# Optimization experiments

Measured on AMD Instinct MI355X. Metric: run time of the kernel, lower is better.

Reference implementation:

```python
import math
import jax, jax.numpy as jnp
from jax import lax
import numpy as np

B, C, H, W = 2, 48, 64, 64
DI, DS, DCONV, DTR = 96, 16, 4, 3   # d_inner=expand*dim, d_state, d_conv, dt_rank=ceil(48/16)
HF = 96                              # SEFN hidden = dim * ffn_expansion_factor(2)


def _posenc(L, d):
    pos = jnp.arange(L, dtype=jnp.float32)[:, None]
    div = jnp.exp(jnp.arange(0, d, 2, dtype=jnp.float32) * (-math.log(10000.0) / d))
    pe = jnp.zeros((L, d), jnp.float32)
    pe = pe.at[:, 0::2].set(jnp.sin(pos * div))
    pe = pe.at[:, 1::2].set(jnp.cos(pos * div))
    return pe


def _ln(x, w, b, eps=1e-5):  # last-dim LayerNorm, biased variance (torch unbiased=False)
    mu = x.mean(-1, keepdims=True)
    var = ((x - mu) ** 2).mean(-1, keepdims=True)
    return (x - mu) / jnp.sqrt(var + eps) * w + b


def _ln4d(x, w, b):  # WithBias LayerNorm over channel dim of NCHW (to_3d/to_4d round trip)
    b_, c_, h_, w_ = x.shape
    xf = x.reshape(b_, c_, h_ * w_).transpose(0, 2, 1)
    return _ln(xf, w, b).transpose(0, 2, 1).reshape(b_, c_, h_, w_)


def _flip_odd(x):  # flip last axis on odd rows of axis -2 (snake reordering)
    return x.at[:, :, 1::2, :].set(x[:, :, 1::2, ::-1])


def _conv2d(x, w, bias=None, groups=1, pad=0):
    y = lax.conv_general_dilated(x, w, (1, 1), [(pad, pad), (pad, pad)],
                                 feature_group_count=groups,
                                 dimension_numbers=('NCHW', 'OIHW', 'NCHW'))
    if bias is not None:
        y = y + bias[None, :, None, None]
    return y


def _mamba(x, inproj, convw, convb, xproj, dtw, dtb, Alog, D, outproj):
    # standard mamba_ssm Mamba forward; x: (B, L, C)
    b_, L, _ = x.shape
    xz = x @ inproj.T                      # (B, L, 2*DI)
    xm, z = xz[..., :DI], xz[..., DI:]
    xc = xm.transpose(0, 2, 1)             # (B, DI, L)
    xc = lax.conv_general_dilated(xc, convw, (1,), [(DCONV - 1, 0)],
                                  feature_group_count=DI,
                                  dimension_numbers=('NCH', 'OIH', 'NCH'))
    xc = jax.nn.silu(xc + convb[None, :, None]).transpose(0, 2, 1)  # (B, L, DI)
    x_dbl = xc @ xproj.T                   # (B, L, DTR + 2*DS)
    dt = jax.nn.softplus(x_dbl[..., :DTR] @ dtw.T + dtb)            # (B, L, DI)
    Bm = x_dbl[..., DTR:DTR + DS]          # (B, L, DS)
    Cm = x_dbl[..., DTR + DS:]             # (B, L, DS)
    A = -jnp.exp(Alog)                     # (DI, DS)
    dA = jnp.exp(dt[..., None] * A)        # (B, L, DI, DS)
    dBx = dt[..., None] * Bm[:, :, None, :] * xc[..., None]

    def step(h, t):
        dA_t, dBx_t, C_t = t
        h = dA_t * h + dBx_t
        return h, jnp.einsum('bds,bs->bd', h, C_t)

    h0 = jnp.zeros((b_, DI, DS), x.dtype)
    _, ys = lax.scan(step, h0, (dA.transpose(1, 0, 2, 3), dBx.transpose(1, 0, 2, 3), Cm.transpose(1, 0, 2)))
    y = ys.transpose(1, 0, 2) + xc * D
    y = y * jax.nn.silu(z)
    return y @ outproj.T


def _forward(x, n1_w, n1_b, n2_w, n2_b, mln1_w, mln1_b, mln2_w, mln2_b,
             m1, m2, f_pin, f_dw, f_fus, f_dwa, f_pout,
             f_c1w, f_c1b, f_ln1_w, f_ln1_b, f_c2w, f_c2b, f_ln2_w, f_ln2_b):
    x_spatial = x
    L = H * W
    pe = _posenc(L, C)
    # --- MambaLayer: bidirectional flip-scan ---
    xn = _ln4d(x, n1_w, n1_b)
    rev1 = _flip_odd(xn)                               # snake order over rows
    rev2 = _flip_odd(xn.transpose(0, 1, 3, 2))         # snake order over cols
    x1_flat = rev1.reshape(B, C, L).transpose(0, 2, 1) + pe
    x2_flat = rev2.reshape(B, C, L).transpose(0, 2, 1) + pe
    y1 = _mamba(_ln(x1_flat, mln1_w, mln1_b), *m1)
    y2 = _mamba(_ln(x2_flat, mln2_w, mln2_b), *m2)
    out1 = _flip_odd(y1.transpose(0, 2, 1).reshape(B, C, H, W))
    out2 = _flip_odd(y2.transpose(0, 2, 1).reshape(B, C, W, H)).transpose(0, 1, 3, 2)
    x = x + out1 + out2
    # --- SEFN ---
    xn2 = _ln4d(x, n2_w, n2_b)
    xp = _conv2d(xn2, f_pin)                           # (B, 2*HF, H, W)
    y = x_spatial.reshape(B, C, H // 2, 2, W // 2, 2).mean((3, 5))   # AvgPool2d(2)
    y = jax.nn.relu(_ln4d(_conv2d(y, f_c1w, f_c1b, pad=1), f_ln1_w, f_ln1_b))
    y = jax.nn.relu(_ln4d(_conv2d(y, f_c2w, f_c2b, pad=1), f_ln2_w, f_ln2_b))
    y = jnp.repeat(jnp.repeat(y, 2, axis=2), 2, axis=3)              # nearest Upsample(2)
    xd = _conv2d(xp, f_dw, groups=2 * HF, pad=1)
    x1, x2 = xd[:, :HF], xd[:, HF:]
    x1 = _conv2d(jnp.concatenate([x1, y], axis=1), f_fus)
    x1 = _conv2d(x1, f_dwa, groups=HF, pad=1)
    ff = _conv2d(jax.nn.gelu(x1, approximate=False) * x2, f_pout)
    return x + ff


def setup_inputs():
    key = jax.random.key(0)
    ks = iter(jax.random.split(key, 64))

    def nrm(shape, s):
        return s * jax.random.normal(next(ks), shape, jnp.float32)

    inp = {}
    inp['x'] = nrm((B, C, H, W), 1.0)
    for nm in ['n1', 'n2', 'mln1', 'mln2', 'f_ln1', 'f_ln2']:
        inp[nm + '_w'] = jnp.ones((C,), jnp.float32)
        inp[nm + '_b'] = jnp.zeros((C,), jnp.float32)
    for p in ['m1', 'm2']:
        inp[p + '_inproj'] = nrm((2 * DI, C), 0.1)
        inp[p + '_convw'] = nrm((DI, 1, DCONV), 0.3)
        inp[p + '_convb'] = jnp.zeros((DI,), jnp.float32)
        inp[p + '_xproj'] = nrm((DTR + 2 * DS, DI), 0.1)
        inp[p + '_dtw'] = nrm((DI, DTR), 0.3)
        u = jax.random.uniform(next(ks), (DI,), jnp.float32)
        inp[p + '_dtb'] = jnp.log(jnp.expm1(0.001 + 0.099 * u))  # mamba dt bias init
        inp[p + '_Alog'] = jnp.log(jnp.tile(jnp.arange(1., DS + 1., dtype=jnp.float32), (DI, 1)))
        inp[p + '_D'] = jnp.ones((DI,), jnp.float32)
        inp[p + '_outproj'] = nrm((C, DI), 0.1)
    inp['f_pin'] = nrm((2 * HF, C, 1, 1), 0.1)
    inp['f_dw'] = nrm((2 * HF, 1, 3, 3), 0.2)
    inp['f_fus'] = nrm((HF, HF + C, 1, 1), 0.08)
    inp['f_dwa'] = nrm((HF, 1, 3, 3), 0.2)
    inp['f_pout'] = nrm((C, HF, 1, 1), 0.1)
    inp['f_c1w'] = nrm((C, C, 3, 3), 0.05)
    inp['f_c1b'] = jnp.zeros((C,), jnp.float32)
    inp['f_c2w'] = nrm((C, C, 3, 3), 0.05)
    inp['f_c2b'] = jnp.zeros((C,), jnp.float32)
    return inp


def reference(x, n1_w, n1_b, n2_w, n2_b, mln1_w, mln1_b, mln2_w, mln2_b,
              m1_inproj, m1_convw, m1_convb, m1_xproj, m1_dtw, m1_dtb, m1_Alog, m1_D, m1_outproj,
              m2_inproj, m2_convw, m2_convb, m2_xproj, m2_dtw, m2_dtb, m2_Alog, m2_D, m2_outproj,
              f_pin, f_dw, f_fus, f_dwa, f_pout,
              f_c1w, f_c1b, f_ln1_w, f_ln1_b, f_c2w, f_c2b, f_ln2_w, f_ln2_b):
    m1 = (m1_inproj, m1_convw, m1_convb, m1_xproj, m1_dtw, m1_dtb, m1_Alog, m1_D, m1_outproj)
    m2 = (m2_inproj, m2_convw, m2_convb, m2_xproj, m2_dtw, m2_dtb, m2_Alog, m2_D, m2_outproj)
    return _forward(x, n1_w, n1_b, n2_w, n2_b, mln1_w, mln1_b, mln2_w, mln2_b,
                    m1, m2, f_pin, f_dw, f_fus, f_dwa, f_pout,
                    f_c1w, f_c1b, f_ln1_w, f_ln1_b, f_c2w, f_c2b, f_ln2_w, f_ln2_b)
```

## Files before the change

### kernel.cpp

```cpp
#include <hip/hip_runtime.h>

#define DEV __device__ __forceinline__

DEV float siluf(float x){ return x / (1.f + __expf(-x)); }
DEV float softplusf(float x){ return fmaxf(x, 0.f) + log1pf(expf(-fabsf(x))); }
DEV float geluf(float x){ return 0.5f * x * (1.f + erff(x * 0.70710678118654752440f)); }

__global__ __launch_bounds__(256) void kA_front(const float* __restrict__ x,
    const float* __restrict__ n1w, const float* __restrict__ n1b,
    const float* __restrict__ mw0, const float* __restrict__ mb0,
    const float* __restrict__ mw1, const float* __restrict__ mb1,
    const float* __restrict__ ip0, const float* __restrict__ ip1,
    float* __restrict__ xmg, float* __restrict__ Vg){
  __shared__ alignas(16) float Vl[48*36];
  __shared__ float Wt[48*97];
  __shared__ float mu_s[32], rs_s[32];
  int bd = blockIdx.x >> 7, tile = blockIdx.x & 127;
  int dir = bd >> 1, b = bd & 1;
  int t0 = tile*32;
  int tid = threadIdx.x;
  const float* ip = dir ? ip1 : ip0;
  const float* mw = dir ? mw1 : mw0;
  const float* mb = dir ? mb1 : mb0;
  for (int i = tid; i < 96*48; i += 256){
    int j = i / 48, c = i % 48;
    Wt[c*97 + j] = ip[i];
  }
  for (int i = tid; i < 48*32; i += 256){
    int c = i >> 5, r = i & 31;
    int t = t0 + r;
    int h, w;
    if (dir == 0){ h = t >> 6; int wp = t & 63; w = (h & 1) ? 63 - wp : wp; }
    else         { w = t >> 6; int hp = t & 63; h = (w & 1) ? 63 - hp : hp; }
    Vl[c*36 + r] = x[(size_t)b*48*4096 + c*4096 + h*64 + w];
  }
  __syncthreads();
  {
    int r = tid >> 3, k = tid & 7;
    float s1 = 0.f, s2 = 0.f;
    #pragma unroll
    for (int cc = 0; cc < 6; cc++){
      float v = Vl[(k*6+cc)*36 + r];
      s1 += v; s2 += v*v;
    }
    s1 += __shfl_xor(s1,1); s2 += __shfl_xor(s2,1);
    s1 += __shfl_xor(s1,2); s2 += __shfl_xor(s2,2);
    s1 += __shfl_xor(s1,4); s2 += __shfl_xor(s2,4);
    if (k == 0){
      float m = s1*(1.f/48.f);
      mu_s[r] = m;
      rs_s[r] = rsqrtf(s2*(1.f/48.f) - m*m + 1e-5f);
    }
  }
  __syncthreads();
  for (int i = tid; i < 32*48; i += 256){
    int r = i / 48, c = i % 48;
    int t = t0 + r;
    float v = Vl[c*36 + r];
    float xn = (v - mu_s[r])*rs_s[r]*n1w[c] + n1b[c];
    float ang = (float)t * __expf(-(float)(c & ~1) * (9.210340371976184f/48.f));
    float pe = (c & 1) ? cosf(ang) : sinf(ang);
    Vl[c*36 + r] = xn + pe;
  }
  __syncthreads();
  {
    int r = tid >> 3, k = tid & 7;
    float s1 = 0.f, s2 = 0.f;
    #pragma unroll
    for (int cc = 0; cc < 6; cc++){
      float v = Vl[(k*6+cc)*36 + r];
      s1 += v; s2 += v*v;
    }
    s1 += __shfl_xor(s1,1); s2 += __shfl_xor(s2,1);
    s1 += __shfl_xor(s1,2); s2 += __shfl_xor(s2,2);
    s1 += __shfl_xor(s1,4); s2 += __shfl_xor(s2,4);
    if (k == 0){
      float m = s1*(1.f/48.f);
      mu_s[r] = m;
      rs_s[r] = rsqrtf(s2*(1.f/48.f) - m*m + 1e-5f);
    }
  }
  __syncthreads();
  for (int i = tid; i < 32*48; i += 256){
    int r = i / 48, c = i % 48;
    float v = Vl[c*36 + r];
    float v2 = (v - mu_s[r])*rs_s[r]*mw[c] + mb[c];
    Vl[c*36 + r] = v2;
    Vg[((size_t)bd*4096 + t0 + r)*48 + c] = v2;
  }
  __syncthreads();
  for (int k = 0; k < 3; k++){
    int i = tid + k*256;
    int j = i % 96, rb = i / 96;
    float a0=0.f, a1=0.f, a2=0.f, a3=0.f;
    #pragma unroll 4
    for (int c = 0; c < 48; c++){
      float wv = Wt[c*97 + j];
      const float4 v4 = *(const float4*)&Vl[c*36 + rb*4];
      a0 += wv*v4.x; a1 += wv*v4.y; a2 += wv*v4.z; a3 += wv*v4.w;
    }
    size_t g = ((size_t)bd*4096 + t0 + rb*4)*96 + j;
    xmg[g] = a0; xmg[g+96] = a1; xmg[g+192] = a2; xmg[g+288] = a3;
  }
}

__global__ __launch_bounds__(384) void kB_convscan(const float* __restrict__ xmg,
    const float* __restrict__ cwp0, const float* __restrict__ cwp1,
    const float* __restrict__ cbp0, const float* __restrict__ cbp1,
    const float* __restrict__ xpp0, const float* __restrict__ xpp1,
    const float* __restrict__ dwp0, const float* __restrict__ dwp1,
    const float* __restrict__ dbp0, const float* __restrict__ dbp1,
    const float* __restrict__ Alog0, const float* __restrict__ Alog1,
    float* __restrict__ xcg, float* __restrict__ dtg,
    float* __restrict__ Bmg, float* __restrict__ Cmg,
    float* __restrict__ P, float* __restrict__ S){
  __shared__ union UB {
    float xml[96*36];
    struct { float xwl[35*96]; float xdbl[35*33]; } p;
  } ub;
  __shared__ float xcl[96*33];
  __shared__ float dtl[96*33];
  __shared__ alignas(16) float Bl[32*16], Cl[32*16];
  __shared__ float cw[96*4], cbv[96], dwl[96*3], dbl[96];
  int bd = blockIdx.x >> 7, tile = blockIdx.x & 127;
  int dir = bd >> 1;
  int t0 = tile*32;
  int tid = threadIdx.x;
  const float* cwp = dir ? cwp1 : cwp0;
  const float* cbp = dir ? cbp1 : cbp0;
  const float* xpp = dir ? xpp1 : xpp0;
  const float* dwp = dir ? dwp1 : dwp0;
  const float* dbp = dir ? dbp1 : dbp0;
  const float* Alog = dir ? Alog1 : Alog0;
  for (int i = tid; i < 35*96; i += 384){
    int tl = i / 96, d = i % 96;
    int t = t0 - 3 + tl;
    ub.xml[d*36 + tl] = (t >= 0) ? xmg[((size_t)bd*4096 + t)*96 + d] : 0.f;
  }
  for (int i = tid; i < 96*4;  i += 384) cw[i] = cwp[i];
  for (int i = tid; i < 96*3;  i += 384) dwl[i] = dwp[i];
  for (int i = tid; i < 96;    i += 384){ cbv[i] = cbp[i]; dbl[i] = dbp[i]; }
  __syncthreads();
  for (int i = tid; i < 96*32; i += 384){
    int d = i >> 5, t = i & 31;
    float acc = cbv[d];
    #pragma unroll
    for (int k = 0; k < 4; k++) acc += cw[d*4+k]*ub.xml[d*36 + t + k];
    xcl[d*33 + t] = siluf(acc);
  }
  __syncthreads();
  for (int i = tid; i < 35*96; i += 384) ub.p.xwl[i] = xpp[i];
  __syncthreads();
  for (int i = tid; i < 35*32; i += 384){
    int j = i / 32, t = i % 32;
    float acc = 0.f;
    #pragma unroll 4
    for (int d = 0; d < 96; d++) acc += xcl[d*33 + t]*ub.p.xwl[j*96 + d];
    ub.p.xdbl[j*33 + t] = acc;
  }
  __syncthreads();
  for (int i = tid; i < 96*32; i += 384){
    int d = i >> 5, t = i & 31;
    float v = dbl[d];
    #pragma unroll
    for (int r = 0; r < 3; r++) v += ub.p.xdbl[r*33 + t]*dwl[d*3 + r];
    dtl[d*33 + t] = softplusf(v);
  }
  for (int i = tid; i < 32*16; i += 384){
    int t = i / 16, s = i % 16;
    Bl[t*16 + s] = ub.p.xdbl[(3+s)*33 + t];
    Cl[t*16 + s] = ub.p.xdbl[(19+s)*33 + t];
  }
  __syncthreads();
  for (int i = tid; i < 32*96; i += 384){
    int t = i / 96, d = i % 96;
    size_t g = ((size_t)bd*4096 + t0 + t)*96 + d;
    xcg[g] = xcl[d*33 + t];
    dtg[g] = dtl[d*33 + t];
  }
  for (int i = tid; i < 32*16; i += 384){
    int t = i / 16, s = i % 16;
    size_t g = ((size_t)bd*4096 + t0 + t)*16 + s;
    Bmg[g] = Bl[t*16 + s];
    Cmg[g] = Cl[t*16 + s];
  }
  {
    int d = tid >> 2, q = tid & 3;
    float A0 = -__expf(Alog[d*16 + q*4 + 0]);
    float A1 = -__expf(Alog[d*16 + q*4 + 1]);
    float A2 = -__expf(Alog[d*16 + q*4 + 2]);
    float A3 = -__expf(Alog[d*16 + q*4 + 3]);
    float h0=0.f,h1=0.f,h2=0.f,h3=0.f, p0=1.f,p1=1.f,p2=1.f,p3=1.f;
    #pragma unroll 4
    for (int t = 0; t < 32; t++){
      float dtd = dtl[d*33 + t];
      float u = dtd * xcl[d*33 + t];
      const float4 b4 = *(const float4*)&Bl[t*16 + q*4];
      float a0 = __expf(dtd*A0), a1 = __expf(dtd*A1), a2 = __expf(dtd*A2), a3 = __expf(dtd*A3);
      h0 = a0*h0 + u*b4.x; p0 *= a0;
      h1 = a1*h1 + u*b4.y; p1 *= a1;
      h2 = a2*h2 + u*b4.z; p2 *= a2;
      h3 = a3*h3 + u*b4.w; p3 *= a3;
    }
    size_t ob = (size_t)blockIdx.x*1536 + d*16 + q*4;
    *(float4*)&P[ob] = make_float4(p0,p1,p2,p3);
    *(float4*)&S[ob] = make_float4(h0,h1,h2,h3);
  }
}

__global__ __launch_bounds__(256) void k4_comb(float* __restrict__ P, const float* __restrict__ S){
  int tid2 = blockIdx.x*256 + threadIdx.x;
  int bd = tid2 / 1536, r = tid2 % 1536;
  size_t idx = (size_t)bd*128*1536 + r;
  const int ST = 1536;
  float pb0,pb1,pb2,pb3,pb4,pb5,pb6,pb7, sb0,sb1,sb2,sb3,sb4,sb5,sb6,sb7;
  pb0=P[idx+0*ST]; sb0=S[idx+0*ST]; pb1=P[idx+1*ST]; sb1=S[idx+1*ST];
  pb2=P[idx+2*ST]; sb2=S[idx+2*ST]; pb3=P[idx+3*ST]; sb3=S[idx+3*ST];
  pb4=P[idx+4*ST]; sb4=S[idx+4*ST]; pb5=P[idx+5*ST]; sb5=S[idx+5*ST];
  pb6=P[idx+6*ST]; sb6=S[idx+6*ST]; pb7=P[idx+7*ST]; sb7=S[idx+7*ST];
  float h = 0.f;
  for (int c0 = 0; c0 < 128; c0 += 8){
    float pn0=0,sn0=0,pn1=0,sn1=0,pn2=0,sn2=0,pn3=0,sn3=0;
    float pn4=0,sn4=0,pn5=0,sn5=0,pn6=0,sn6=0,pn7=0,sn7=0;
    if (c0 + 8 < 128){
      pn0=P[idx+(size_t)(c0+8)*ST];  sn0=S[idx+(size_t)(c0+8)*ST];
      pn1=P[idx+(size_t)(c0+9)*ST];  sn1=S[idx+(size_t)(c0+9)*ST];
      pn2=P[idx+(size_t)(c0+10)*ST]; sn2=S[idx+(size_t)(c0+10)*ST];
      pn3=P[idx+(size_t)(c0+11)*ST]; sn3=S[idx+(size_t)(c0+11)*ST];
      pn4=P[idx+(size_t)(c0+12)*ST]; sn4=S[idx+(size_t)(c0+12)*ST];
      pn5=P[idx+(size_t)(c0+13)*ST]; sn5=S[idx+(size_t)(c0+13)*ST];
      pn6=P[idx+(size_t)(c0+14)*ST]; sn6=S[idx+(size_t)(c0+14)*ST];
      pn7=P[idx+(size_t)(c0+15)*ST]; sn7=S[idx+(size_t)(c0+15)*ST];
    }
    P[idx+(size_t)(c0+0)*ST] = h; h = pb0*h + sb0;
    P[idx+(size_t)(c0+1)*ST] = h; h = pb1*h + sb1;
    P[idx+(size_t)(c0+2)*ST] = h; h = pb2*h + sb2;
    P[idx+(size_t)(c0+3)*ST] = h; h = pb3*h + sb3;
    P[idx+(size_t)(c0+4)*ST] = h; h = pb4*h + sb4;
    P[idx+(size_t)(c0+5)*ST] = h; h = pb5*h + sb5;
    P[idx+(size_t)(c0+6)*ST] = h; h = pb6*h + sb6;
    P[idx+(size_t)(c0+7)*ST] = h; h = pb7*h + sb7;
    pb0=pn0;sb0=sn0;pb1=pn1;sb1=sn1;pb2=pn2;sb2=sn2;pb3=pn3;sb3=sn3;
    pb4=pn4;sb4=sn4;pb5=pn5;sb5=sn5;pb6=pn6;sb6=sn6;pb7=pn7;sb7=sn7;
  }
}

__global__ __launch_bounds__(384) void k5_scan2(const float* __restrict__ dtg,
    const float* __restrict__ xcg, const float* __restrict__ Bmg, const float* __restrict__ Cmg,
    const float* __restrict__ Alog0, const float* __restrict__ Alog1,
    const float* __restrict__ Dp0, const float* __restrict__ Dp1,
    const float* __restrict__ ip0, const float* __restrict__ ip1,
    const float* __restrict__ Vg, const float* __restrict__ Hin, float* __restrict__ yout){
  __shared__ union U5 {
    struct { float dts[32*96]; float xcs[32*96]; } s;
    struct { float Wzt[48*96]; float Vgs[32*48]; } e;
  } u;
  __shared__ alignas(16) float Bl[32*16], Cl[32*16];
  __shared__ float yl[32*96];
  int task = blockIdx.x;
  int bd = task >> 7, ch = task & 127;
  int t0 = ch*32;
  int tid = threadIdx.x;
  const float* ip   = (bd >= 2) ? ip1 : ip0;
  const float* Alog = (bd >= 2) ? Alog1 : Alog0;
  const float* Dp   = (bd >= 2) ? Dp1 : Dp0;
  for (int i = tid; i < 32*96; i += 384){
    int t = i / 96, dd = i % 96;
    size_t g = ((size_t)bd*4096 + t0 + t)*96 + dd;
    u.s.dts[i] = dtg[g];
    u.s.xcs[i] = xcg[g];
  }
  for (int i = tid; i < 32*16; i += 384){
    size_t g = ((size_t)bd*4096 + t0)*16 + i;
    Bl[i] = Bmg[g];
    Cl[i] = Cmg[g];
  }
  __syncthreads();
  {
    int d = tid >> 2, q = tid & 3;
    float A0 = -__expf(Alog[d*16 + q*4 + 0]);
    float A1 = -__expf(Alog[d*16 + q*4 + 1]);
    float A2 = -__expf(Alog[d*16 + q*4 + 2]);
    float A3 = -__expf(Alog[d*16 + q*4 + 3]);
    float Dd = Dp[d];
    const float4 h4 = *(const float4*)&Hin[(size_t)task*1536 + d*16 + q*4];
    float h0 = h4.x, h1 = h4.y, h2 = h4.z, h3 = h4.w;
    for (int t = 0; t < 32; t += 2){
      float dtdA = u.s.dts[t*96 + d];
      float xcvA = u.s.xcs[t*96 + d];
// ... 69 lines not shown
    if (pass == 0){
      for (int i = tid; i < 16*96; i += 384){
        int wl_ = i / 96, d = i % 96;
        int wsp = w0 + wl_;
        int wp = (h & 1) ? 63 - wsp : wsp;
        ul.ylds[wl_*97 + d] = y[((size_t)b*4096 + h*64 + wp)*96 + d];
      }
    } else {
      for (int i = tid; i < 16*96; i += 384){
        int wl_ = i / 96, d = i % 96;
        int wsp = w0 + wl_;
        int t = wsp*64 + ((wsp & 1) ? 63 - h : h);
        ul.ylds[wl_*97 + d] = y[((size_t)b*4096 + t)*96 + d];
      }
    }
    __syncthreads();
    #pragma unroll 4
    for (int d = 0; d < 96; d++){
      float yv = ul.ylds[w*97 + d];
      acc0 += yv * bufW[(cg*2+0)*97 + d];
      acc1 += yv * bufW[(cg*2+1)*97 + d];
    }
  }
  __syncthreads();
  {
    int c0 = cg*2;
    size_t idx0 = (((size_t)b*48 + c0)*64 + h)*64 + w0 + w;
    float v0 = x[idx0] + acc0;
    xmid[idx0] = v0;
    ul.l.xl[c0*17 + w] = v0;
    size_t idx1 = idx0 + 4096;
    float v1 = x[idx1] + acc1;
    xmid[idx1] = v1;
    ul.l.xl[(c0+1)*17 + w] = v1;
  }
  for (int i = tid; i < 192*48; i += 384){
    int r = i / 48, c = i % 48;
    bufW[r*49 + c] = pin[i];
  }
  __syncthreads();
  if (tid < 128){
    int r = tid >> 3, k = tid & 7;
    float s1 = 0.f, s2 = 0.f;
    #pragma unroll
    for (int cc = 0; cc < 6; cc++){
      float v = ul.l.xl[(k*6+cc)*17 + r];
      s1 += v; s2 += v*v;
    }
    s1 += __shfl_xor(s1,1); s2 += __shfl_xor(s2,1);
    s1 += __shfl_xor(s1,2); s2 += __shfl_xor(s2,2);
    s1 += __shfl_xor(s1,4); s2 += __shfl_xor(s2,4);
    if (k == 0){
      float m = s1*(1.f/48.f);
      ul.l.mu[r] = m;
      ul.l.rs[r] = rsqrtf(s2*(1.f/48.f) - m*m + 1e-5f);
    }
  }
  __syncthreads();
  for (int i = tid; i < 48*16; i += 384){
    int c = i >> 4, ww = i & 15;
    ul.l.xl[c*17 + ww] = (ul.l.xl[c*17 + ww] - ul.l.mu[ww])*ul.l.rs[ww]*nw[c] + nb[c];
  }
  __syncthreads();
  for (int it = 0; it < 2; it++){
    int i = tid + it*384;
    int ww = i & 15, oq = i >> 4;
    int o0 = oq*4;
    float a0=0,a1=0,a2=0,a3=0;
    #pragma unroll 4
    for (int c = 0; c < 48; c++){
      float xv = ul.l.xl[c*17 + ww];
      a0 += xv*bufW[(o0+0)*49 + c];
      a1 += xv*bufW[(o0+1)*49 + c];
      a2 += xv*bufW[(o0+2)*49 + c];
      a3 += xv*bufW[(o0+3)*49 + c];
    }
    xp[(((size_t)b*192 + o0+0)*64 + h)*64 + w0 + ww] = a0;
    xp[(((size_t)b*192 + o0+1)*64 + h)*64 + w0 + ww] = a1;
    xp[(((size_t)b*192 + o0+2)*64 + h)*64 + w0 + ww] = a2;
    xp[(((size_t)b*192 + o0+3)*64 + h)*64 + w0 + ww] = a3;
  }
}

__global__ __launch_bounds__(384) void k9_conv3(const float* __restrict__ in,
    const float* __restrict__ wgt, const float* __restrict__ bias,
    const float* __restrict__ lnw, const float* __restrict__ lnb,
    float* __restrict__ out, int pooled, int lnin){
  __shared__ float wl[12*48*9];
  __shared__ float sin_[48*3*34];
  __shared__ float mu_i[104], rs_i[104];
  int bid = blockIdx.x;
  int cq = bid & 3, i0 = (bid >> 2) & 31, b = bid >> 7;
  int tid = threadIdx.x;
  for (int i = tid; i < 12*48*9; i += 384) wl[i] = wgt[cq*12*48*9 + i];
  for (int i = tid; i < 48*3*34; i += 384){
    int jx = i % 34, ky = (i/34) % 3, ci = i/102;
    int r = i0 + ky - 1, j = jx - 1;
    float v = 0.f;
    if (r >= 0 && r < 32 && j >= 0 && j < 32){
      if (pooled){
        const float* xb = in + (((size_t)b*48 + ci)*64 + 2*r)*64 + 2*j;
        v = 0.25f*(xb[0] + xb[1] + xb[64] + xb[65]);
      } else {
        v = in[(((size_t)b*48 + ci)*32 + r)*32 + j];
      }
    }
    sin_[i] = v;
  }
  __syncthreads();
  if (lnin){
    if (tid < 102){
      int jx = tid % 34, ky = tid / 34;
      int r = i0 + ky - 1, j = jx - 1;
      if (r >= 0 && r < 32 && j >= 0 && j < 32){
        float s1 = 0.f, s2 = 0.f;
        #pragma unroll 4
        for (int ci = 0; ci < 48; ci++){ float v = sin_[ci*102 + tid]; s1 += v; s2 += v*v; }
        float m = s1*(1.f/48.f);
        mu_i[tid] = m;
        rs_i[tid] = rsqrtf(s2*(1.f/48.f) - m*m + 1e-5f);
      }
    }
    __syncthreads();
    for (int i = tid; i < 48*102; i += 384){
      int ci = i / 102, p = i % 102;
      int jx = p % 34, ky = p / 34;
      int r = i0 + ky - 1, j = jx - 1;
      if (r >= 0 && r < 32 && j >= 0 && j < 32){
        float v = (sin_[i] - mu_i[p])*rs_i[p]*lnw[ci] + lnb[ci];
        sin_[i] = fmaxf(v, 0.f);
      }
    }
    __syncthreads();
  }
  int j = tid & 31, col = tid >> 5;
  float acc = bias[cq*12 + col];
  for (int ci = 0; ci < 48; ci++){
    const float* wp = wl + ((size_t)col*48 + ci)*9;
    const float* sp = sin_ + ci*102;
    #pragma unroll
    for (int ky = 0; ky < 3; ky++)
      #pragma unroll
      for (int kx = 0; kx < 3; kx++)
        acc += sp[ky*34 + j + kx] * wp[ky*3 + kx];
  }
  out[(((size_t)b*48 + cq*12 + col)*32 + i0)*32 + j] = acc;
}

__global__ __launch_bounds__(256) void k13_dw(const float* __restrict__ in,
    const float* __restrict__ wgt, float* __restrict__ out, int CH){
  int idx = blockIdx.x*256 + threadIdx.x;
  if (idx >= 2*CH*1024) return;
  int wq = idx & 15, h = (idx >> 4) & 63, c = (idx >> 10) % CH, b = idx / (CH*1024);
  int w0 = wq*4;
  const float* ip = in + ((size_t)b*CH + c)*4096;
  const float* wp = wgt + c*9;
  float a0=0.f,a1=0.f,a2=0.f,a3=0.f;
  #pragma unroll
  for (int ky = 0; ky < 3; ky++){
    int hh = h + ky - 1;
    if (hh < 0 || hh > 63) continue;
    const float* rp = ip + hh*64;
    float v0 = (w0 > 0)  ? rp[w0-1] : 0.f;
    float v1 = rp[w0+0], v2 = rp[w0+1], v3 = rp[w0+2], v4 = rp[w0+3];
    float v5 = (w0 < 60) ? rp[w0+4] : 0.f;
    float k0 = wp[ky*3+0], k1 = wp[ky*3+1], k2 = wp[ky*3+2];
    a0 += k0*v0 + k1*v1 + k2*v2;
    a1 += k0*v1 + k1*v2 + k2*v3;
    a2 += k0*v2 + k1*v3 + k2*v4;
    a3 += k0*v3 + k1*v4 + k2*v5;
  }
  float* op = out + (((size_t)b*CH + c)*64 + h)*64 + w0;
  op[0]=a0; op[1]=a1; op[2]=a2; op[3]=a3;
}

__global__ __launch_bounds__(256) void k14_fus(const float* __restrict__ xd,
    const float* __restrict__ cv2, const float* __restrict__ lnw, const float* __restrict__ lnb,
    const float* __restrict__ fus, float* __restrict__ x1){
  __shared__ float wl[48*144];
  __shared__ float al[96][64];
  __shared__ float yl[48][32];
  __shared__ float muy[32], rsy[32];
  int bid = blockIdx.x;
  int oh = bid & 1, h = (bid >> 1) & 63, b = bid >> 7;
  int tid = threadIdx.x;
  for (int i = tid; i < 48*144; i += 256) wl[i] = fus[(size_t)oh*48*144 + i];
  for (int i = tid; i < 96*64; i += 256){
    int ci = i >> 6, w = i & 63;
    al[ci][w] = xd[(((size_t)b*192 + ci)*64 + h)*64 + w];
  }
  for (int i = tid; i < 48*32; i += 256){
    int cj = i >> 5, j = i & 31;
    yl[cj][j] = cv2[(((size_t)b*48 + cj)*32 + (h >> 1))*32 + j];
  }
  __syncthreads();
  if (tid < 32){
    float s1 = 0.f, s2 = 0.f;
    #pragma unroll 4
    for (int cj = 0; cj < 48; cj++){ float v = yl[cj][tid]; s1 += v; s2 += v*v; }
    float m = s1*(1.f/48.f);
    muy[tid] = m;
    rsy[tid] = rsqrtf(s2*(1.f/48.f) - m*m + 1e-5f);
  }
  __syncthreads();
  for (int i = tid; i < 48*32; i += 256){
    int cj = i >> 5, j = i & 31;
    yl[cj][j] = fmaxf((yl[cj][j] - muy[j])*rsy[j]*lnw[cj] + lnb[cj], 0.f);
  }
  __syncthreads();
  for (int it = 0; it < 3; it++){
    int i = tid + it*256;
    int w = i & 63, ob = i >> 6; int o0 = ob*4;
    float a[4] = {0,0,0,0};
    #pragma unroll 4
    for (int ci = 0; ci < 96; ci++){
      float xv = al[ci][w];
      #pragma unroll
      for (int q = 0; q < 4; q++) a[q] += xv * wl[(o0+q)*144 + ci];
    }
    int w2 = w >> 1;
    #pragma unroll 4
    for (int cj = 0; cj < 48; cj++){
      float yv = yl[cj][w2];
      #pragma unroll
      for (int q = 0; q < 4; q++) a[q] += yv * wl[(o0+q)*144 + 96 + cj];
    }
    #pragma unroll
    for (int q = 0; q < 4; q++)
      x1[(((size_t)b*96 + oh*48 + o0 + q)*64 + h)*64 + w] = a[q];
  }
}
// ... 20 lines not shown
    float v = 0.f;
    if (hh >= 0 && hh < 64 && ww_ >= 0 && ww_ < 64)
      v = x1[(((size_t)b*96 + ch)*64 + hh)*64 + ww_];
    xs[i] = v;
  }
  __syncthreads();
  for (int i = tid; i < 96*16; i += 384){
    int ch = i >> 4, ww = i & 15;
    const float* wp = dwl + ch*9;
    const float* sp = xs + ch*54;
    float a = 0.f;
    #pragma unroll
    for (int ky = 0; ky < 3; ky++)
      #pragma unroll
      for (int kx = 0; kx < 3; kx++)
        a += sp[ky*18 + ww + kx] * wp[ky*3 + kx];
    float x2 = xd[(((size_t)b*192 + 96 + ch)*64 + h)*64 + w0 + ww];
    gl[ch*17 + ww] = geluf(a) * x2;
  }
  __syncthreads();
  int ww = tid & 15, cg = tid >> 4;
  float a0=0.f, a1=0.f;
  #pragma unroll 4
  for (int ch = 0; ch < 96; ch++){
    float gv = gl[ch*17 + ww];
    a0 += gv * wl[(cg*2+0)*97 + ch];
    a1 += gv * wl[(cg*2+1)*97 + ch];
  }
  {
    int c0 = cg*2;
    size_t idx0 = (((size_t)b*48 + c0)*64 + h)*64 + w0 + ww;
    out[idx0] = xmid[idx0] + a0;
    size_t idx1 = idx0 + 4096;
    out[idx1] = xmid[idx1] + a1;
  }
}

extern "C" void kernel_launch(void* const* d_in, const int* in_sizes, int n_in,
                              void* d_out, int out_size, void* d_ws, size_t ws_size,
                              hipStream_t stream){
  (void)in_sizes; (void)n_in; (void)out_size; (void)ws_size;
  const float* x    = (const float*)d_in[0];
  const float* n1w  = (const float*)d_in[1];
  const float* n1b  = (const float*)d_in[2];
  const float* n2w  = (const float*)d_in[3];
  const float* n2b  = (const float*)d_in[4];
  const float* mlnw[2] = {(const float*)d_in[5], (const float*)d_in[7]};
  const float* mlnb[2] = {(const float*)d_in[6], (const float*)d_in[8]};
  const float* fln1w = (const float*)d_in[9];
  const float* fln1b = (const float*)d_in[10];
  const float* fln2w = (const float*)d_in[11];
  const float* fln2b = (const float*)d_in[12];
  const float* inproj[2]  = {(const float*)d_in[13], (const float*)d_in[22]};
  const float* convw[2]   = {(const float*)d_in[14], (const float*)d_in[23]};
  const float* convb[2]   = {(const float*)d_in[15], (const float*)d_in[24]};
  const float* xproj[2]   = {(const float*)d_in[16], (const float*)d_in[25]};
  const float* dtw[2]     = {(const float*)d_in[17], (const float*)d_in[26]};
  const float* dtbp[2]    = {(const float*)d_in[18], (const float*)d_in[27]};
  const float* Alog[2]    = {(const float*)d_in[19], (const float*)d_in[28]};
  const float* Dp[2]      = {(const float*)d_in[20], (const float*)d_in[29]};
  const float* outproj[2] = {(const float*)d_in[21], (const float*)d_in[30]};
  const float* fpin  = (const float*)d_in[31];
  const float* fdw   = (const float*)d_in[32];
  const float* ffus  = (const float*)d_in[33];
  const float* fdwa  = (const float*)d_in[34];
  const float* fpout = (const float*)d_in[35];
  const float* fc1w  = (const float*)d_in[36];
  const float* fc1b  = (const float*)d_in[37];
  const float* fc2w  = (const float*)d_in[38];
  const float* fc2b  = (const float*)d_in[39];

  float* ws = (float*)d_ws;
  float* xmg = ws + 0;
  float* Vgb = ws + 1572864;
  float* xcg = ws + 2359296;
  float* dtg = ws + 3932160;
  float* Bmg = ws + 5505024;
  float* Cmg = ws + 5767168;
  float* Pb  = ws + 6029312;
  float* Sb  = ws + 6815744;
  float* xmid= ws + 7602176;
  float* yall = xmg;
  float* Hin  = Pb;
  float* ta   = Sb;
  float* tbuf = Sb + 98304;
  float* xpb  = xcg;
  float* xdb  = dtg;
  float* x1b  = Pb;

  kA_front<<<512,256,0,stream>>>(x, n1w, n1b,
      mlnw[0], mlnb[0], mlnw[1], mlnb[1], inproj[0], inproj[1], xmg, Vgb);
  kB_convscan<<<512,384,0,stream>>>(xmg,
      convw[0], convw[1], convb[0], convb[1], xproj[0], xproj[1],
      dtw[0], dtw[1], dtbp[0], dtbp[1], Alog[0], Alog[1],
      xcg, dtg, Bmg, Cmg, Pb, Sb);
  k4_comb  <<<24,256,0,stream>>>(Pb, Sb);
  k5_scan2 <<<512,384,0,stream>>>(dtg, xcg, Bmg, Cmg, Alog[0], Alog[1],
      Dp[0], Dp[1], inproj[0], inproj[1], Vgb, Hin, yall);
  k67_mid  <<<512,384,0,stream>>>(x, yall, yall + 786432, outproj[0], outproj[1],
      n2w, n2b, fpin, xmid, xpb);
  k9_conv3 <<<256,384,0,stream>>>(x,  fc1w, fc1b, fln1w, fln1b, ta,   1, 0);
  k9_conv3 <<<256,384,0,stream>>>(ta, fc2w, fc2b, fln1w, fln1b, tbuf, 0, 1);
  k13_dw   <<<1536,256,0,stream>>>(xpb, fdw, xdb, 192);
  k14_fus  <<<256,256,0,stream>>>(xdb, tbuf, fln2w, fln2b, ffus, x1b);
  k16_out  <<<512,384,0,stream>>>(x1b, xdb, fdwa, fpout, xmid, (float*)d_out);
}
```

Measured before the change: 184.8 us.

## Merge independent SEFN 3x3 conv branches into the Mamba front kernels

The two 3x3 conv launches on the pooled spatial branch are folded into the Mamba front and conv-scan kernels as extra blocks selected by block index, since they are independent of the Mamba path. This removes two kernel launches and lets the small 256-block conv work overlap with the 512-block Mamba stages. Their intermediate buffers now live in the output buffer instead of the workspace. Shared memory is unioned across roles, and the conv1 branch runs with 256 threads and loops over its 384 outputs.

```diff
diff --git a/kernel.cpp b/kernel.cpp
--- a/kernel.cpp
+++ b/kernel.cpp
@@ -6,205 +6,291 @@
 DEV float softplusf(float x){ return fmaxf(x, 0.f) + log1pf(expf(-fabsf(x))); }
 DEV float geluf(float x){ return 0.5f * x * (1.f + erff(x * 0.70710678118654752440f)); }
 
-__global__ __launch_bounds__(256) void kA_front(const float* __restrict__ x,
+__global__ __launch_bounds__(256) void kA9(const float* __restrict__ x,
     const float* __restrict__ n1w, const float* __restrict__ n1b,
     const float* __restrict__ mw0, const float* __restrict__ mb0,
     const float* __restrict__ mw1, const float* __restrict__ mb1,
     const float* __restrict__ ip0, const float* __restrict__ ip1,
-    float* __restrict__ xmg, float* __restrict__ Vg){
-  __shared__ alignas(16) float Vl[48*36];
-  __shared__ float Wt[48*97];
-  __shared__ float mu_s[32], rs_s[32];
-  int bd = blockIdx.x >> 7, tile = blockIdx.x & 127;
-  int dir = bd >> 1, b = bd & 1;
-  int t0 = tile*32;
+    const float* __restrict__ fc1w, const float* __restrict__ fc1b,
+    float* __restrict__ xmg, float* __restrict__ Vg, float* __restrict__ ta){
+  __shared__ union alignas(16) UA {
+    struct { float Vl[48*36]; float Wt[48*97]; float mu_s[32]; float rs_s[32]; } a;
+    struct { float wl[12*48*9]; float sin_[48*102]; } c;
+  } u;
   int tid = threadIdx.x;
-  const float* ip = dir ? ip1 : ip0;
-  const float* mw = dir ? mw1 : mw0;
-  const float* mb = dir ? mb1 : mb0;
-  for (int i = tid; i < 96*48; i += 256){
-    int j = i / 48, c = i % 48;
-    Wt[c*97 + j] = ip[i];
-  }
-  for (int i = tid; i < 48*32; i += 256){
-    int c = i >> 5, r = i & 31;
-    int t = t0 + r;
-    int h, w;
-    if (dir == 0){ h = t >> 6; int wp = t & 63; w = (h & 1) ? 63 - wp : wp; }
-    else         { w = t >> 6; int hp = t & 63; h = (w & 1) ? 63 - hp : hp; }
-    Vl[c*36 + r] = x[(size_t)b*48*4096 + c*4096 + h*64 + w];
-  }
-  __syncthreads();
-  {
-    int r = tid >> 3, k = tid & 7;
-    float s1 = 0.f, s2 = 0.f;
-    #pragma unroll
-    for (int cc = 0; cc < 6; cc++){
-      float v = Vl[(k*6+cc)*36 + r];
-      s1 += v; s2 += v*v;
-    }
-    s1 += __shfl_xor(s1,1); s2 += __shfl_xor(s2,1);
-    s1 += __shfl_xor(s1,2); s2 += __shfl_xor(s2,2);
-    s1 += __shfl_xor(s1,4); s2 += __shfl_xor(s2,4);
-    if (k == 0){
-      float m = s1*(1.f/48.f);
-      mu_s[r] = m;
-      rs_s[r] = rsqrtf(s2*(1.f/48.f) - m*m + 1e-5f);
-    }
-  }
-  __syncthreads();
-  for (int i = tid; i < 32*48; i += 256){
-    int r = i / 48, c = i % 48;
-    int t = t0 + r;
-    float v = Vl[c*36 + r];
-    float xn = (v - mu_s[r])*rs_s[r]*n1w[c] + n1b[c];
-    float ang = (float)t * __expf(-(float)(c & ~1) * (9.210340371976184f/48.f));
-    float pe = (c & 1) ? cosf(ang) : sinf(ang);
-    Vl[c*36 + r] = xn + pe;
-  }
-  __syncthreads();
-  {
-    int r = tid >> 3, k = tid & 7;
-    float s1 = 0.f, s2 = 0.f;
-    #pragma unroll
-    for (int cc = 0; cc < 6; cc++){
-      float v = Vl[(k*6+cc)*36 + r];
-      s1 += v; s2 += v*v;
-    }
-    s1 += __shfl_xor(s1,1); s2 += __shfl_xor(s2,1);
-    s1 += __shfl_xor(s1,2); s2 += __shfl_xor(s2,2);
-    s1 += __shfl_xor(s1,4); s2 += __shfl_xor(s2,4);
-    if (k == 0){
-      float m = s1*(1.f/48.f);
-      mu_s[r] = m;
-      rs_s[r] = rsqrtf(s2*(1.f/48.f) - m*m + 1e-5f);
-    }
-  }
-  __syncthreads();
-  for (int i = tid; i < 32*48; i += 256){
-    int r = i / 48, c = i % 48;
-    float v = Vl[c*36 + r];
-    float v2 = (v - mu_s[r])*rs_s[r]*mw[c] + mb[c];
-    Vl[c*36 + r] = v2;
-    Vg[((size_t)bd*4096 + t0 + r)*48 + c] = v2;
-  }
-  __syncthreads();
-  for (int k = 0; k < 3; k++){
-    int i = tid + k*256;
-    int j = i % 96, rb = i / 96;
-    float a0=0.f, a1=0.f, a2=0.f, a3=0.f;
-    #pragma unroll 4
-    for (int c = 0; c < 48; c++){
-      float wv = Wt[c*97 + j];
-      const float4 v4 = *(const float4*)&Vl[c*36 + rb*4];
-      a0 += wv*v4.x; a1 += wv*v4.y; a2 += wv*v4.z; a3 += wv*v4.w;
-    }
-    size_t g = ((size_t)bd*4096 + t0 + rb*4)*96 + j;
-    xmg[g] = a0; xmg[g+96] = a1; xmg[g+192] = a2; xmg[g+288] = a3;
-  }
-}
-
-__global__ __launch_bounds__(384) void kB_convscan(const float* __restrict__ xmg,
+  if (blockIdx.x < 512){
+    int bd = blockIdx.x >> 7, tile = blockIdx.x & 127;
+    int dir = bd >> 1, b = bd & 1;
+    int t0 = tile*32;
+    const float* ip = dir ? ip1 : ip0;
+    const float* mw = dir ? mw1 : mw0;
+    const float* mb = dir ? mb1 : mb0;
+    for (int i = tid; i < 96*48; i += 256){
+      int j = i / 48, c = i % 48;
+      u.a.Wt[c*97 + j] = ip[i];
+    }
+    for (int i = tid; i < 48*32; i += 256){
+      int c = i >> 5, r = i & 31;
+      int t = t0 + r;
+      int h, w;
+      if (dir == 0){ h = t >> 6; int wp = t & 63; w = (h & 1) ? 63 - wp : wp; }
+      else         { w = t >> 6; int hp = t & 63; h = (w & 1) ? 63 - hp : hp; }
+      u.a.Vl[c*36 + r] = x[(size_t)b*48*4096 + c*4096 + h*64 + w];
+    }
+    __syncthreads();
+    {
+      int r = tid >> 3, k = tid & 7;
+      float s1 = 0.f, s2 = 0.f;
+      #pragma unroll
+      for (int cc = 0; cc < 6; cc++){
+        float v = u.a.Vl[(k*6+cc)*36 + r];
+        s1 += v; s2 += v*v;
+      }
+      s1 += __shfl_xor(s1,1); s2 += __shfl_xor(s2,1);
+      s1 += __shfl_xor(s1,2); s2 += __shfl_xor(s2,2);
+      s1 += __shfl_xor(s1,4); s2 += __shfl_xor(s2,4);
+      if (k == 0){
+        float m = s1*(1.f/48.f);
+        u.a.mu_s[r] = m;
+        u.a.rs_s[r] = rsqrtf(s2*(1.f/48.f) - m*m + 1e-5f);
+      }
+    }
+    __syncthreads();
+    for (int i = tid; i < 32*48; i += 256){
+      int r = i / 48, c = i % 48;
+      int t = t0 + r;
+      float v = u.a.Vl[c*36 + r];
+      float xn = (v - u.a.mu_s[r])*u.a.rs_s[r]*n1w[c] + n1b[c];
+      float ang = (float)t * __expf(-(float)(c & ~1) * (9.210340371976184f/48.f));
+      float pe = (c & 1) ? cosf(ang) : sinf(ang);
+      u.a.Vl[c*36 + r] = xn + pe;
+    }
+    __syncthreads();
+    {
+      int r = tid >> 3, k = tid & 7;
+      float s1 = 0.f, s2 = 0.f;
+      #pragma unroll
+      for (int cc = 0; cc < 6; cc++){
+        float v = u.a.Vl[(k*6+cc)*36 + r];
+        s1 += v; s2 += v*v;
+      }
+      s1 += __shfl_xor(s1,1); s2 += __shfl_xor(s2,1);
+      s1 += __shfl_xor(s1,2); s2 += __shfl_xor(s2,2);
+      s1 += __shfl_xor(s1,4); s2 += __shfl_xor(s2,4);
+      if (k == 0){
+        float m = s1*(1.f/48.f);
+        u.a.mu_s[r] = m;
+        u.a.rs_s[r] = rsqrtf(s2*(1.f/48.f) - m*m + 1e-5f);
+      }
+    }
+    __syncthreads();
+    for (int i = tid; i < 32*48; i += 256){
+      int r = i / 48, c = i % 48;
+      float v = u.a.Vl[c*36 + r];
+      float v2 = (v - u.a.mu_s[r])*u.a.rs_s[r]*mw[c] + mb[c];
+      u.a.Vl[c*36 + r] = v2;
+      Vg[((size_t)bd*4096 + t0 + r)*48 + c] = v2;
+    }
+    __syncthreads();
+    for (int k = 0; k < 3; k++){
+      int i = tid + k*256;
+      int j = i % 96, rb = i / 96;
+      float a0=0.f, a1=0.f, a2=0.f, a3=0.f;
+      #pragma unroll 4
+      for (int c = 0; c < 48; c++){
+        float wv = u.a.Wt[c*97 + j];
+        const float4 v4 = *(const float4*)&u.a.Vl[c*36 + rb*4];
+        a0 += wv*v4.x; a1 += wv*v4.y; a2 += wv*v4.z; a3 += wv*v4.w;
+      }
+      size_t g = ((size_t)bd*4096 + t0 + rb*4)*96 + j;
+      xmg[g] = a0; xmg[g+96] = a1; xmg[g+192] = a2; xmg[g+288] = a3;
+    }
+  } else {
+    int bid = blockIdx.x - 512;
+    int cq = bid & 3, i0 = (bid >> 2) & 31, b2 = bid >> 7;
+    for (int i = tid; i < 12*48*9; i += 256) u.c.wl[i] = fc1w[cq*12*48*9 + i];
+    for (int i = tid; i < 48*102; i += 256){
+      int jx = i % 34, ky = (i/34) % 3, ci = i/102;
+      int r = i0 + ky - 1, j = jx - 1;
+      float v = 0.f;
+      if (r >= 0 && r < 32 && j >= 0 && j < 32){
+        const float* xb = x + (((size_t)b2*48 + ci)*64 + 2*r)*64 + 2*j;
+        v = 0.25f*(xb[0] + xb[1] + xb[64] + xb[65]);
+      }
+      u.c.sin_[i] = v;
+    }
+    __syncthreads();
+    for (int i = tid; i < 12*32; i += 256){
+      int j = i & 31, col = i >> 5;
+      float acc = fc1b[cq*12 + col];
+      for (int ci = 0; ci < 48; ci++){
+        const float* wp = u.c.wl + ((size_t)col*48 + ci)*9;
+        const float* sp = u.c.sin_ + ci*102;
+        #pragma unroll
+        for (int ky = 0; ky < 3; ky++)
+          #pragma unroll
+          for (int kx = 0; kx < 3; kx++)
+            acc += sp[ky*34 + j + kx] * wp[ky*3 + kx];
+      }
+      ta[(((size_t)b2*48 + cq*12 + col)*32 + i0)*32 + j] = acc;
+    }
+  }
+}
+
+__global__ __launch_bounds__(384) void kB9(const float* __restrict__ xmg,
     const float* __restrict__ cwp0, const float* __restrict__ cwp1,
     const float* __restrict__ cbp0, const float* __restrict__ cbp1,
     const float* __restrict__ xpp0, const float* __restrict__ xpp1,
     const float* __restrict__ dwp0, const float* __restrict__ dwp1,
     const float* __restrict__ dbp0, const float* __restrict__ dbp1,
     const float* __restrict__ Alog0, const float* __restrict__ Alog1,
+    const float* __restrict__ ta, const float* __restrict__ fc2w, const float* __restrict__ fc2b,
+    const float* __restrict__ fln1w, const float* __restrict__ fln1b,
     float* __restrict__ xcg, float* __restrict__ dtg,
     float* __restrict__ Bmg, float* __restrict__ Cmg,
-    float* __restrict__ P, float* __restrict__ S){
-  __shared__ union UB {
-    float xml[96*36];
-    struct { float xwl[35*96]; float xdbl[35*33]; } p;
-  } ub;
-  __shared__ float xcl[96*33];
-  __shared__ float dtl[96*33];
-  __shared__ alignas(16) float Bl[32*16], Cl[32*16];
-  __shared__ float cw[96*4], cbv[96], dwl[96*3], dbl[96];
-  int bd = blockIdx.x >> 7, tile = blockIdx.x & 127;
-  int dir = bd >> 1;
-  int t0 = tile*32;
+    float* __restrict__ P, float* __restrict__ S, float* __restrict__ tbuf){
+  __shared__ union alignas(16) UBB {
+    struct {
+      float Bl[32*16]; float Cl[32*16];
+      union { float xml[96*36]; struct { float xwl[35*96]; float xdbl[35*33]; } p; } ub;
+      float xcl[96*33]; float dtl[96*33];
+      float cw[96*4]; float cbv[96]; float dwl[96*3]; float dbl[96];
+    } b;
+    struct { float wl[12*48*9]; float sin_[48*102]; float mu_i[104]; float rs_i[104]; } c;
+  } u;
   int tid = threadIdx.x;
-  const float* cwp = dir ? cwp1 : cwp0;
-  const float* cbp = dir ? cbp1 : cbp0;
-  const float* xpp = dir ? xpp1 : xpp0;
-  const float* dwp = dir ? dwp1 : dwp0;
-  const float* dbp = dir ? dbp1 : dbp0;
-  const float* Alog = dir ? Alog1 : Alog0;
-  for (int i = tid; i < 35*96; i += 384){
-    int tl = i / 96, d = i % 96;
-    int t = t0 - 3 + tl;
-    ub.xml[d*36 + tl] = (t >= 0) ? xmg[((size_t)bd*4096 + t)*96 + d] : 0.f;
-  }
-  for (int i = tid; i < 96*4;  i += 384) cw[i] = cwp[i];
-  for (int i = tid; i < 96*3;  i += 384) dwl[i] = dwp[i];
-  for (int i = tid; i < 96;    i += 384){ cbv[i] = cbp[i]; dbl[i] = dbp[i]; }
-  __syncthreads();
-  for (int i = tid; i < 96*32; i += 384){
-    int d = i >> 5, t = i & 31;
-    float acc = cbv[d];
-    #pragma unroll
-    for (int k = 0; k < 4; k++) acc += cw[d*4+k]*ub.xml[d*36 + t + k];
-    xcl[d*33 + t] = siluf(acc);
-  }
-  __syncthreads();
-  for (int i = tid; i < 35*96; i += 384) ub.p.xwl[i] = xpp[i];
-  __syncthreads();
-  for (int i = tid; i < 35*32; i += 384){
-    int j = i / 32, t = i % 32;
-    float acc = 0.f;
-    #pragma unroll 4
-    for (int d = 0; d < 96; d++) acc += xcl[d*33 + t]*ub.p.xwl[j*96 + d];
-    ub.p.xdbl[j*33 + t] = acc;
-  }
-  __syncthreads();
-  for (int i = tid; i < 96*32; i += 384){
-    int d = i >> 5, t = i & 31;
-    float v = dbl[d];
-    #pragma unroll
-    for (int r = 0; r < 3; r++) v += ub.p.xdbl[r*33 + t]*dwl[d*3 + r];
-    dtl[d*33 + t] = softplusf(v);
-  }
-  for (int i = tid; i < 32*16; i += 384){
-    int t = i / 16, s = i % 16;
-    Bl[t*16 + s] = ub.p.xdbl[(3+s)*33 + t];
-    Cl[t*16 + s] = ub.p.xdbl[(19+s)*33 + t];
-  }
-  __syncthreads();
-  for (int i = tid; i < 32*96; i += 384){
-    int t = i / 96, d = i % 96;
-    size_t g = ((size_t)bd*4096 + t0 + t)*96 + d;
-    xcg[g] = xcl[d*33 + t];
-    dtg[g] = dtl[d*33 + t];
-  }
-  for (int i = tid; i < 32*16; i += 384){
-    int t = i / 16, s = i % 16;
-    size_t g = ((size_t)bd*4096 + t0 + t)*16 + s;
-    Bmg[g] = Bl[t*16 + s];
-    Cmg[g] = Cl[t*16 + s];
-  }
-  {
-    int d = tid >> 2, q = tid & 3;
-    float A0 = -__expf(Alog[d*16 + q*4 + 0]);
-    float A1 = -__expf(Alog[d*16 + q*4 + 1]);
-    float A2 = -__expf(Alog[d*16 + q*4 + 2]);
-    float A3 = -__expf(Alog[d*16 + q*4 + 3]);
-    float h0=0.f,h1=0.f,h2=0.f,h3=0.f, p0=1.f,p1=1.f,p2=1.f,p3=1.f;
-    #pragma unroll 4
-    for (int t = 0; t < 32; t++){
-      float dtd = dtl[d*33 + t];
-      float u = dtd * xcl[d*33 + t];
-      const float4 b4 = *(const float4*)&Bl[t*16 + q*4];
-      float a0 = __expf(dtd*A0), a1 = __expf(dtd*A1), a2 = __expf(dtd*A2), a3 = __expf(dtd*A3);
-      h0 = a0*h0 + u*b4.x; p0 *= a0;
-      h1 = a1*h1 + u*b4.y; p1 *= a1;
-      h2 = a2*h2 + u*b4.z; p2 *= a2;
-      h3 = a3*h3 + u*b4.w; p3 *= a3;
-    }
-    size_t ob = (size_t)blockIdx.x*1536 + d*16 + q*4;
-    *(float4*)&P[ob] = make_float4(p0,p1,p2,p3);
-    *(float4*)&S[ob] = make_float4(h0,h1,h2,h3);
+  if (blockIdx.x < 512){
+    int bd = blockIdx.x >> 7, tile = blockIdx.x & 127;
+    int dir = bd >> 1;
+    int t0 = tile*32;
+    const float* cwp = dir ? cwp1 : cwp0;
+    const float* cbp = dir ? cbp1 : cbp0;
+    const float* xpp = dir ? xpp1 : xpp0;
+    const float* dwp = dir ? dwp1 : dwp0;
+    const float* dbp = dir ? dbp1 : dbp0;
+    const float* Alog = dir ? Alog1 : Alog0;
+    for (int i = tid; i < 35*96; i += 384){
+      int tl = i / 96, d = i % 96;
+      int t = t0 - 3 + tl;
+      u.b.ub.xml[d*36 + tl] = (t >= 0) ? xmg[((size_t)bd*4096 + t)*96 + d] : 0.f;
+    }
+    for (int i = tid; i < 96*4;  i += 384) u.b.cw[i] = cwp[i];
+    for (int i = tid; i < 96*3;  i += 384) u.b.dwl[i] = dwp[i];
+    for (int i = tid; i < 96;    i += 384){ u.b.cbv[i] = cbp[i]; u.b.dbl[i] = dbp[i]; }
+    __syncthreads();
+    for (int i = tid; i < 96*32; i += 384){
+      int d = i >> 5, t = i & 31;
+      float acc = u.b.cbv[d];
+      #pragma unroll
+      for (int k = 0; k < 4; k++) acc += u.b.cw[d*4+k]*u.b.ub.xml[d*36 + t + k];
+      u.b.xcl[d*33 + t] = siluf(acc);
+    }
+    __syncthreads();
+    for (int i = tid; i < 35*96; i += 384) u.b.ub.p.xwl[i] = xpp[i];
+    __syncthreads();
+    for (int i = tid; i < 35*32; i += 384){
+      int j = i / 32, t = i % 32;
+      float acc = 0.f;
+      #pragma unroll 4
+      for (int d = 0; d < 96; d++) acc += u.b.xcl[d*33 + t]*u.b.ub.p.xwl[j*96 + d];
+      u.b.ub.p.xdbl[j*33 + t] = acc;
+    }
+    __syncthreads();
+    for (int i = tid; i < 96*32; i += 384){
+      int d = i >> 5, t = i & 31;
+      float v = u.b.dbl[d];
+      #pragma unroll
+      for (int r = 0; r < 3; r++) v += u.b.ub.p.xdbl[r*33 + t]*u.b.dwl[d*3 + r];
+      u.b.dtl[d*33 + t] = softplusf(v);
+    }
+    for (int i = tid; i < 32*16; i += 384){
+      int t = i / 16, s = i % 16;
+      u.b.Bl[t*16 + s] = u.b.ub.p.xdbl[(3+s)*33 + t];
+      u.b.Cl[t*16 + s] = u.b.ub.p.xdbl[(19+s)*33 + t];
+    }
+    __syncthreads();
+    for (int i = tid; i < 32*96; i += 384){
+      int t = i / 96, d = i % 96;
+      size_t g = ((size_t)bd*4096 + t0 + t)*96 + d;
+      xcg[g] = u.b.xcl[d*33 + t];
+      dtg[g] = u.b.dtl[d*33 + t];
+    }
+    for (int i = tid; i < 32*16; i += 384){
+      int t = i / 16, s = i % 16;
+      size_t g = ((size_t)bd*4096 + t0 + t)*16 + s;
+      Bmg[g] = u.b.Bl[t*16 + s];
+      Cmg[g] = u.b.Cl[t*16 + s];
+    }
+    {
+      int d = tid >> 2, q = tid & 3;
+      float A0 = -__expf(Alog[d*16 + q*4 + 0]);
+      float A1 = -__expf(Alog[d*16 + q*4 + 1]);
+      float A2 = -__expf(Alog[d*16 + q*4 + 2]);
+      float A3 = -__expf(Alog[d*16 + q*4 + 3]);
+      float h0=0.f,h1=0.f,h2=0.f,h3=0.f, p0=1.f,p1=1.f,p2=1.f,p3=1.f;
+      #pragma unroll 4
+      for (int t = 0; t < 32; t++){
+        float dtd = u.b.dtl[d*33 + t];
+        float uu = dtd * u.b.xcl[d*33 + t];
+        const float4 b4 = *(const float4*)&u.b.Bl[t*16 + q*4];
+        float a0 = __expf(dtd*A0), a1 = __expf(dtd*A1), a2 = __expf(dtd*A2), a3 = __expf(dtd*A3);
+        h0 = a0*h0 + uu*b4.x; p0 *= a0;
+        h1 = a1*h1 + uu*b4.y; p1 *= a1;
+        h2 = a2*h2 + uu*b4.z; p2 *= a2;
+        h3 = a3*h3 + uu*b4.w; p3 *= a3;
+      }
+      size_t ob = (size_t)blockIdx.x*1536 + d*16 + q*4;
+      *(float4*)&P[ob] = make_float4(p0,p1,p2,p3);
+      *(float4*)&S[ob] = make_float4(h0,h1,h2,h3);
+    }
+  } else {
+    int bid = blockIdx.x - 512;
+    int cq = bid & 3, i0 = (bid >> 2) & 31, b2 = bid >> 7;
+    for (int i = tid; i < 12*48*9; i += 384) u.c.wl[i] = fc2w[cq*12*48*9 + i];
+    for (int i = tid; i < 48*102; i += 384){
+      int jx = i % 34, ky = (i/34) % 3, ci = i/102;
+      int r = i0 + ky - 1, j = jx - 1;
+      float v = 0.f;
+      if (r >= 0 && r < 32 && j >= 0 && j < 32)
+        v = ta[(((size_t)b2*48 + ci)*32 + r)*32 + j];
+      u.c.sin_[i] = v;
+    }
+    __syncthreads();
+    if (tid < 102){
+      int jx = tid % 34, ky = tid / 34;
+      int r = i0 + ky - 1, j = jx - 1;
+      if (r >= 0 && r < 32 && j >= 0 && j < 32){
+        float s1 = 0.f, s2 = 0.f;
+        #pragma unroll 4
+        for (int ci = 0; ci < 48; ci++){ float v = u.c.sin_[ci*102 + tid]; s1 += v; s2 += v*v; }
+        float m = s1*(1.f/48.f);
+        u.c.mu_i[tid] = m;
+        u.c.rs_i[tid] = rsqrtf(s2*(1.f/48.f) - m*m + 1e-5f);
+      }
+    }
+    __syncthreads();
+    for (int i = tid; i < 48*102; i += 384){
+      int ci = i / 102, p = i % 102;
+      int jx = p % 34, ky = p / 34;
+      int r = i0 + ky - 1, j = jx - 1;
+      if (r >= 0 && r < 32 && j >= 0 && j < 32){
+        float v = (u.c.sin_[i] - u.c.mu_i[p])*u.c.rs_i[p]*fln1w[ci] + fln1b[ci];
+        u.c.sin_[i] = fmaxf(v, 0.f);
+      }
+    }
+    __syncthreads();
+    int j = tid & 31, col = tid >> 5;
+    float acc = fc2b[cq*12 + col];
+    for (int ci = 0; ci < 48; ci++){
+      const float* wp = u.c.wl + ((size_t)col*48 + ci)*9;
+      const float* sp = u.c.sin_ + ci*102;
+      #pragma unroll
+      for (int ky = 0; ky < 3; ky++)
+        #pragma unroll
+        for (int kx = 0; kx < 3; kx++)
+          acc += sp[ky*34 + j + kx] * wp[ky*3 + kx];
+    }
+    tbuf[(((size_t)b2*48 + cq*12 + col)*32 + i0)*32 + j] = acc;
   }
 }
 
@@ -440,71 +526,6 @@
   }
 }
 
-__global__ __launch_bounds__(384) void k9_conv3(const float* __restrict__ in,
-    const float* __restrict__ wgt, const float* __restrict__ bias,
-    const float* __restrict__ lnw, const float* __restrict__ lnb,
-    float* __restrict__ out, int pooled, int lnin){
-  __shared__ float wl[12*48*9];
-  __shared__ float sin_[48*3*34];
-  __shared__ float mu_i[104], rs_i[104];
-  int bid = blockIdx.x;
-  int cq = bid & 3, i0 = (bid >> 2) & 31, b = bid >> 7;
-  int tid = threadIdx.x;
-  for (int i = tid; i < 12*48*9; i += 384) wl[i] = wgt[cq*12*48*9 + i];
-  for (int i = tid; i < 48*3*34; i += 384){
-    int jx = i % 34, ky = (i/34) % 3, ci = i/102;
-    int r = i0 + ky - 1, j = jx - 1;
-    float v = 0.f;
-    if (r >= 0 && r < 32 && j >= 0 && j < 32){
-      if (pooled){
-        const float* xb = in + (((size_t)b*48 + ci)*64 + 2*r)*64 + 2*j;
-        v = 0.25f*(xb[0] + xb[1] + xb[64] + xb[65]);
-      } else {
-        v = in[(((size_t)b*48 + ci)*32 + r)*32 + j];
-      }
-    }
-    sin_[i] = v;
-  }
-  __syncthreads();
-  if (lnin){
-    if (tid < 102){
-      int jx = tid % 34, ky = tid / 34;
-      int r = i0 + ky - 1, j = jx - 1;
-      if (r >= 0 && r < 32 && j >= 0 && j < 32){
-        float s1 = 0.f, s2 = 0.f;
-        #pragma unroll 4
-        for (int ci = 0; ci < 48; ci++){ float v = sin_[ci*102 + tid]; s1 += v; s2 += v*v; }
-        float m = s1*(1.f/48.f);
-        mu_i[tid] = m;
-        rs_i[tid] = rsqrtf(s2*(1.f/48.f) - m*m + 1e-5f);
-      }
-    }
-    __syncthreads();
-    for (int i = tid; i < 48*102; i += 384){
-      int ci = i / 102, p = i % 102;
-      int jx = p % 34, ky = p / 34;
-      int r = i0 + ky - 1, j = jx - 1;
-      if (r >= 0 && r < 32 && j >= 0 && j < 32){
-        float v = (sin_[i] - mu_i[p])*rs_i[p]*lnw[ci] + lnb[ci];
-        sin_[i] = fmaxf(v, 0.f);
-      }
-    }
-    __syncthreads();
-  }
-  int j = tid & 31, col = tid >> 5;
-  float acc = bias[cq*12 + col];
-  for (int ci = 0; ci < 48; ci++){
-    const float* wp = wl + ((size_t)col*48 + ci)*9;
-    const float* sp = sin_ + ci*102;
-    #pragma unroll
-    for (int ky = 0; ky < 3; ky++)
-      #pragma unroll
-      for (int kx = 0; kx < 3; kx++)
-        acc += sp[ky*34 + j + kx] * wp[ky*3 + kx];
-  }
-  out[(((size_t)b*48 + cq*12 + col)*32 + i0)*32 + j] = acc;
-}
-
 __global__ __launch_bounds__(256) void k13_dw(const float* __restrict__ in,
     const float* __restrict__ wgt, float* __restrict__ out, int CH){
   int idx = blockIdx.x*256 + threadIdx.x;
@@ -691,25 +712,26 @@
   float* xmid= ws + 7602176;
   float* yall = xmg;
   float* Hin  = Pb;
-  float* ta   = Sb;
-  float* tbuf = Sb + 98304;
   float* xpb  = xcg;
   float* xdb  = dtg;
   float* x1b  = Pb;
-
-  kA_front<<<512,256,0,stream>>>(x, n1w, n1b,
-      mlnw[0], mlnb[0], mlnw[1], mlnb[1], inproj[0], inproj[1], xmg, Vgb);
-  kB_convscan<<<512,384,0,stream>>>(xmg,
+  float* outf = (float*)d_out;
+  float* ta   = outf;
+  float* tbuf = outf + 98304;
+
+  kA9<<<768,256,0,stream>>>(x, n1w, n1b,
+      mlnw[0], mlnb[0], mlnw[1], mlnb[1], inproj[0], inproj[1],
+      fc1w, fc1b, xmg, Vgb, ta);
+  kB9<<<768,384,0,stream>>>(xmg,
       convw[0], convw[1], convb[0], convb[1], xproj[0], xproj[1],
       dtw[0], dtw[1], dtbp[0], dtbp[1], Alog[0], Alog[1],
-      xcg, dtg, Bmg, Cmg, Pb, Sb);
+      ta, fc2w, fc2b, fln1w, fln1b,
+      xcg, dtg, Bmg, Cmg, Pb, Sb, tbuf);
   k4_comb  <<<24,256,0,stream>>>(Pb, Sb);
   k5_scan2 <<<512,384,0,stream>>>(dtg, xcg, Bmg, Cmg, Alog[0], Alog[1],
       Dp[0], Dp[1], inproj[0], inproj[1], Vgb, Hin, yall);
   k67_mid  <<<512,384,0,stream>>>(x, yall, yall + 786432, outproj[0], outproj[1],
       n2w, n2b, fpin, xmid, xpb);
-  k9_conv3 <<<256,384,0,stream>>>(x,  fc1w, fc1b, fln1w, fln1b, ta,   1, 0);
-  k9_conv3 <<<256,384,0,stream>>>(ta, fc2w, fc2b, fln1w, fln1b, tbuf, 0, 1);
   k13_dw   <<<1536,256,0,stream>>>(xpb, fdw, xdb, 192);
   k14_fus  <<<256,256,0,stream>>>(xdb, tbuf, fln2w, fln2b, ffus, x1b);
   k16_out  <<<512,384,0,stream>>>(x1b, xdb, fdwa, fpout, xmid, (float*)d_out);
```

Result: faster. 167.3 us (-9.5%).
